# Kernel optimization log

Measured on AMD Instinct MI355X. Metric: run time of the kernel, lower is better.

The kernel has to match this reference:

```python
import jax, jax.numpy as jnp
import numpy as np

N = 50000
E = 500000
CH = 256
H1, C1 = 4, 64
H2, C2 = 8, 32
CONCAT = H1 * C1 + H2 * C2  # 512


def setup_inputs() -> dict:
    key = jax.random.key(0)
    ks = jax.random.split(key, 16)
    s = 0.05
    x = jax.random.normal(ks[0], (N, CH), dtype=jnp.float32)
    edge_index = jax.random.randint(ks[1], (2, E), 0, N, dtype=jnp.int64)
    return {
        "x": x,
        "edge_index": edge_index,
        "gamma": jnp.ones((CH,), jnp.float32),
        "beta": jnp.zeros((CH,), jnp.float32),
        "W1": jax.random.normal(ks[2], (CH, H1 * C1), jnp.float32) * s,
        "a_src1": jax.random.normal(ks[3], (H1, C1), jnp.float32) * s,
        "a_dst1": jax.random.normal(ks[4], (H1, C1), jnp.float32) * s,
        "b1": jnp.zeros((H1 * C1,), jnp.float32),
        "W2": jax.random.normal(ks[5], (CH, H2 * C2), jnp.float32) * s,
        "a_src2": jax.random.normal(ks[6], (H2, C2), jnp.float32) * s,
        "a_dst2": jax.random.normal(ks[7], (H2, C2), jnp.float32) * s,
        "b2": jnp.zeros((H2 * C2,), jnp.float32),
        "Wu": jax.random.normal(ks[8], (CONCAT, CH), jnp.float32) * s,
        "bu": jnp.zeros((CH,), jnp.float32),
    }


def _layer_norm(x, gamma, beta, eps=1e-5):
    mu = jnp.mean(x, axis=-1, keepdims=True)
    var = jnp.var(x, axis=-1, keepdims=True)
    return (x - mu) * jax.lax.rsqrt(var + eps) * gamma + beta


def _gat_conv(x, src, dst, W, a_src, a_dst, bias, heads, out_ch, n_nodes):
    # x: [N, CH] -> per-head projection h: [N, H, C]
    h = (x @ W).reshape(n_nodes, heads, out_ch)
    alpha_s = jnp.einsum('nhc,hc->nh', h, a_src)  # [N, H]
    alpha_d = jnp.einsum('nhc,hc->nh', h, a_dst)  # [N, H]
    e = jax.nn.leaky_relu(alpha_s[src] + alpha_d[dst], negative_slope=0.2)  # [E, H]
    # segment softmax over incoming edges of each dst node (self-loops guarantee nonempty segments)
    m = jax.ops.segment_max(e, dst, num_segments=n_nodes)
    ex = jnp.exp(e - m[dst])
    denom = jax.ops.segment_sum(ex, dst, num_segments=n_nodes)
    a = ex / (denom[dst] + 1e-16)  # [E, H]
    msg = h[src] * a[:, :, None]  # [E, H, C]
    out = jax.ops.segment_sum(msg, dst, num_segments=n_nodes)  # [N, H, C]
    return out.reshape(n_nodes, heads * out_ch) + bias


def reference(x, edge_index, gamma, beta, W1, a_src1, a_dst1, b1,
              W2, a_src2, a_dst2, b2, Wu, bu):
    n = x.shape[0]
    # add self-loops (PyG GATConv default)
    loop = jnp.arange(n, dtype=edge_index.dtype)
    src = jnp.concatenate([edge_index[0], loop])
    dst = jnp.concatenate([edge_index[1], loop])

    residual = x
    x_norm = _layer_norm(x, gamma, beta)
    out1 = _gat_conv(x_norm, src, dst, W1, a_src1, a_dst1, b1, H1, C1, n)
    out2 = _gat_conv(x_norm, src, dst, W2, a_src2, a_dst2, b2, H2, C2, n)
    x_cat = jax.nn.elu(jnp.concatenate([out1, out2], axis=-1))
    unified = x_cat @ Wu + bu
    return residual + unified
```

## Files before the change

### kernel.cpp

```cpp
#include <hip/hip_runtime.h>
#include <hip/hip_bf16.h>
#include <math.h>

constexpr int CH = 256;
constexpr int CC = 512;
constexpr int AP = 16;

typedef __bf16 bf16x8 __attribute__((ext_vector_type(8)));
typedef float  f32x4  __attribute__((ext_vector_type(4)));
typedef float  f32x2  __attribute__((ext_vector_type(2)));
typedef int    i32x4  __attribute__((ext_vector_type(4)));
typedef __attribute__((address_space(3))) void lds_void;
typedef __attribute__((address_space(1))) void glb_void;

__device__ inline unsigned short f2bf(float f) {
    union { float f; unsigned u; } v; v.f = f;
    unsigned r = v.u + 0x7FFFu + ((v.u >> 16) & 1u);
    return (unsigned short)(r >> 16);
}

__global__ void fused_pre_kernel(const float* __restrict__ x, const float* __restrict__ gamma,
                                 const float* __restrict__ beta,
                                 const float* __restrict__ W1, const float* __restrict__ W2,
                                 const float* __restrict__ Wu,
                                 unsigned short* __restrict__ xnb,
                                 unsigned short* __restrict__ WT1, unsigned short* __restrict__ WTu,
                                 int* __restrict__ deg, int N, int LNB) {
    int b = blockIdx.x;
    int t = threadIdx.x;
    if (b < LNB) {
        int wid = b * 4 + (t >> 6);
        int lane = t & 63;
        if (wid >= N) return;
        const float4 v = *(const float4*)(x + (size_t)wid * CH + lane * 4);
        float s = v.x + v.y + v.z + v.w;
        float sq = v.x * v.x + v.y * v.y + v.z * v.z + v.w * v.w;
        #pragma unroll
        for (int o = 32; o; o >>= 1) { s += __shfl_xor(s, o); sq += __shfl_xor(sq, o); }
        float mu = s * (1.0f / CH);
        float var = sq * (1.0f / CH) - mu * mu;
        float rs = rsqrtf(var + 1e-5f);
        float4 g = *(const float4*)(gamma + lane * 4);
        float4 bb = *(const float4*)(beta + lane * 4);
        unsigned short o0 = f2bf((v.x - mu) * rs * g.x + bb.x);
        unsigned short o1 = f2bf((v.y - mu) * rs * g.y + bb.y);
        unsigned short o2 = f2bf((v.z - mu) * rs * g.z + bb.z);
        unsigned short o3 = f2bf((v.w - mu) * rs * g.w + bb.w);
        uint2 pk;
        pk.x = (unsigned)o0 | ((unsigned)o1 << 16);
        pk.y = (unsigned)o2 | ((unsigned)o3 << 16);
        *(uint2*)(xnb + (size_t)wid * CH + lane * 4) = pk;
    } else if (b < LNB + 512) {
        int idx = (b - LNB) * 256 + t;
        int n = idx >> 8, k = idx & 255;
        float v = (n < 256) ? W1[(size_t)k * 256 + n] : W2[(size_t)k * 256 + (n - 256)];
        WT1[idx] = f2bf(v);
    } else if (b < LNB + 1024) {
        int idx = (b - LNB - 512) * 256 + t;
        int n = idx >> 9, k = idx & 511;
        WTu[idx] = f2bf(Wu[(size_t)k * 256 + n]);
    } else {
        int i = (b - LNB - 1024) * 256 + t;
        if (i < N) deg[i] = 1;
    }
}

__device__ inline void gemm_core(const unsigned short* __restrict__ Ab,
                                 const unsigned short* __restrict__ Bt,
                                 unsigned short* As, unsigned short* Bs,
                                 f32x4 acc[4][4], int m0, int n0, int M, int K) {
    const int t = threadIdx.x;
    const int lane = t & 63;
    const int wave = t >> 6;
    const int wr = wave >> 1, wc = wave & 1;
    const int srow = lane >> 3;
    const int scol = (((lane & 7) ^ srow) << 3);
    const int fr = lane & 15;
    const int fkb = (lane >> 4) << 4;

    for (int k0 = 0; k0 < K; k0 += 64) {
        __syncthreads();
        #pragma unroll
        for (int c = 0; c < 4; ++c) {
            int chunk = c * 4 + wave;
            int row = chunk * 8 + srow;
            int gra = m0 + row; if (gra >= M) gra = M - 1;
            const unsigned short* ga = Ab + (size_t)gra * K + k0 + scol;
            __builtin_amdgcn_global_load_lds((const glb_void*)ga,
                                             (lds_void*)&As[chunk * 512], 16, 0, 0);
            const unsigned short* gb = Bt + (size_t)(n0 + row) * K + k0 + scol;
            __builtin_amdgcn_global_load_lds((const glb_void*)gb,
                                             (lds_void*)&Bs[chunk * 512], 16, 0, 0);
        }
        __syncthreads();
        #pragma unroll
        for (int ks = 0; ks < 2; ++ks) {
            bf16x8 af[4], bfr[4];
            #pragma unroll
            for (int m = 0; m < 4; ++m) {
                int r = wr * 64 + m * 16 + fr;
                int cb = (ks * 64 + fkb) ^ ((r & 7) << 4);
                af[m] = *(const bf16x8*)((const char*)As + r * 128 + cb);
            }
            #pragma unroll
            for (int n = 0; n < 4; ++n) {
                int r = wc * 64 + n * 16 + fr;
                int cb = (ks * 64 + fkb) ^ ((r & 7) << 4);
                bfr[n] = *(const bf16x8*)((const char*)Bs + r * 128 + cb);
            }
            #pragma unroll
            for (int m = 0; m < 4; ++m)
                #pragma unroll
                for (int n = 0; n < 4; ++n)
                    acc[m][n] = __builtin_amdgcn_mfma_f32_16x16x32_bf16(af[m], bfr[n], acc[m][n], 0, 0, 0);
        }
    }
}

__global__ __launch_bounds__(256) void gemm1_mfma(
    const unsigned short* __restrict__ Ab, const unsigned short* __restrict__ Bt,
    const float* __restrict__ as1, const float* __restrict__ ad1,
    const float* __restrict__ as2, const float* __restrict__ ad2,
    unsigned char* __restrict__ Hq,
    float* __restrict__ alpha_src, float* __restrict__ alpha_dst, int M, int MB) {
    __shared__ unsigned short As[128 * 64];
    __shared__ unsigned short Bs[128 * 64];
    const int s = blockIdx.x;
    const int xcd = s & 7;
    const int jj = s >> 3;
    const int n_blk = jj & 3;
    const int m_blk = (jj >> 2) * 8 + xcd;
    if (m_blk >= MB) return;
    const int m0 = m_blk * 128, n0 = n_blk * 128;
    const int lane = threadIdx.x & 63;
    const int wave = threadIdx.x >> 6;
    const int wr = wave >> 1, wc = wave & 1;
    f32x4 acc[4][4] = {};
    gemm_core(Ab, Bt, As, Bs, acc, m0, n0, M, 256);
    const int fr = lane & 15;
    const int orow = (lane >> 4) * 4;
    #pragma unroll
    for (int m = 0; m < 4; ++m)
        #pragma unroll
        for (int j = 0; j < 4; ++j) {
            int r = m0 + wr * 64 + m * 16 + orow + j;
            if (r < M) {
                #pragma unroll
                for (int n = 0; n < 4; ++n) {
                    int ccol = n0 + wc * 64 + n * 16 + fr;
                    unsigned q = (unsigned)__builtin_amdgcn_cvt_pk_fp8_f32(
                        acc[m][n][j], acc[m][n][j], 0, false) & 0xffu;
                    Hq[(size_t)r * CC + ccol] = (unsigned char)q;
                }
            }
        }
    const int colbase = n0 + wc * 64;
    const bool gat1 = colbase < 256;
    float sv[4], dv[4];
    int headA;
    if (gat1) {
        headA = colbase >> 6;
        #pragma unroll
        for (int n = 0; n < 4; ++n) { int c = colbase + n * 16 + fr; sv[n] = as1[c]; dv[n] = ad1[c]; }
    } else {
        headA = 4 + ((colbase - 256) >> 5);
        #pragma unroll
        for (int n = 0; n < 4; ++n) { int c = colbase - 256 + n * 16 + fr; sv[n] = as2[c]; dv[n] = ad2[c]; }
    }
    #pragma unroll
    for (int m = 0; m < 4; ++m)
        #pragma unroll
        for (int j = 0; j < 4; ++j) {
            int r = m0 + wr * 64 + m * 16 + orow + j;
            float p01s = acc[m][0][j] * sv[0] + acc[m][1][j] * sv[1];
            float p23s = acc[m][2][j] * sv[2] + acc[m][3][j] * sv[3];
            float p01d = acc[m][0][j] * dv[0] + acc[m][1][j] * dv[1];
            float p23d = acc[m][2][j] * dv[2] + acc[m][3][j] * dv[3];
            if (gat1) {
                float ts = p01s + p23s, td = p01d + p23d;
                #pragma unroll
                for (int o = 1; o < 16; o <<= 1) { ts += __shfl_xor(ts, o); td += __shfl_xor(td, o); }
                if (fr == 0 && r < M) {
                    alpha_src[(size_t)r * AP + headA] = ts;
                    alpha_dst[(size_t)r * AP + headA] = td;
                }
            } else {
                #pragma unroll
                for (int o = 1; o < 16; o <<= 1) {
                    p01s += __shfl_xor(p01s, o); p23s += __shfl_xor(p23s, o);
                    p01d += __shfl_xor(p01d, o); p23d += __shfl_xor(p23d, o);
                }
                if (fr == 0 && r < M) {
                    alpha_src[(size_t)r * AP + headA]     = p01s;
                    alpha_dst[(size_t)r * AP + headA]     = p01d;
                    alpha_src[(size_t)r * AP + headA + 1] = p23s;
                    alpha_dst[(size_t)r * AP + headA + 1] = p23d;
                }
            }
        }
}

__global__ __launch_bounds__(256) void gemm2_mfma(const unsigned short* __restrict__ Ab,
                                                  const unsigned short* __restrict__ Bt,
                                                  const float* __restrict__ bu,
                                                  const float* __restrict__ xres,
                                                  float* __restrict__ C, int M, int MB) {
    __shared__ unsigned short As[128 * 64];
    __shared__ unsigned short Bs[128 * 64];
    const int s = blockIdx.x;
    const int xcd = s & 7;
    const int jj = s >> 3;
    const int n_blk = jj & 1;
    const int m_blk = (jj >> 1) * 8 + xcd;
    if (m_blk >= MB) return;
    const int m0 = m_blk * 128, n0 = n_blk * 128;
    const int lane = threadIdx.x & 63;
    const int wave = threadIdx.x >> 6;
    const int wr = wave >> 1, wc = wave & 1;
    f32x4 acc[4][4] = {};
    gemm_core(Ab, Bt, As, Bs, acc, m0, n0, M, 512);
    const int fr = lane & 15;
    const int orow = (lane >> 4) * 4;
    #pragma unroll
    for (int m = 0; m < 4; ++m)
        #pragma unroll
        for (int j = 0; j < 4; ++j) {
            int r = m0 + wr * 64 + m * 16 + orow + j;
            if (r < M) {
                #pragma unroll
                for (int n = 0; n < 4; ++n) {
                    int ccol = n0 + wc * 64 + n * 16 + fr;
                    float xr = __builtin_nontemporal_load(&xres[(size_t)r * CH + ccol]);
                    __builtin_nontemporal_store(acc[m][n][j] + bu[ccol] + xr,
                                                &C[(size_t)r * CH + ccol]);
                }
            }
        }
}

__global__ void hist_kernel(const int* __restrict__ dst, int* __restrict__ deg, int E) {
    int i = blockIdx.x * blockDim.x + threadIdx.x;
    if (i < E) atomicAdd(&deg[dst[i]], 1);
}
__global__ __launch_bounds__(256) void scan1_kernel(const int* __restrict__ deg, int* __restrict__ pre,
                                                    int* __restrict__ bsum, int n) {
    __shared__ int wsum[4];
    int t = threadIdx.x, lane = t & 63, w = t >> 6;
    int base = blockIdx.x * 1024 + t * 4;
    int v0 = base     < n ? deg[base]     : 0;
    int v1 = base + 1 < n ? deg[base + 1] : 0;
    int v2 = base + 2 < n ? deg[base + 2] : 0;
    int v3 = base + 3 < n ? deg[base + 3] : 0;
    int s = v0 + v1 + v2 + v3;
    int sc = s;
    #pragma unroll
    for (int o = 1; o < 64; o <<= 1) { int xx = __shfl_up(sc, o); if (lane >= o) sc += xx; }
    if (lane == 63) wsum[w] = sc;
    __syncthreads();
    int wo = 0;
    #pragma unroll
    for (int k = 0; k < 4; ++k) if (k < w) wo += wsum[k];
    int p = wo + sc - s;
    if (base     < n) pre[base]     = p; p += v0;
    if (base + 1 < n) pre[base + 1] = p; p += v1;
    if (base + 2 < n) pre[base + 2] = p; p += v2;
    if (base + 3 < n) pre[base + 3] = p;
    if (t == 255) bsum[blockIdx.x] = wo + sc;
}
__global__ void scan2_kernel(int* __restrict__ bsum, int nb) {
    int lane = threadIdx.x;
    int v = lane < nb ? bsum[lane] : 0;
    int sc = v;
    #pragma unroll
    for (int o = 1; o < 64; o <<= 1) { int xx = __shfl_up(sc, o); if (lane >= o) sc += xx; }
    if (lane < nb) bsum[lane] = sc - v;
}
__global__ void scan3_csr_kernel(const int* __restrict__ pre, const int* __restrict__ bsum,
                                 int* __restrict__ offsets, int* __restrict__ cursor,
                                 int* __restrict__ csr, int n, int total) {
    int i = blockIdx.x * 256 + threadIdx.x;
    if (i < n) {
        int off = pre[i] + bsum[i >> 10];
        offsets[i] = off;
        cursor[i] = off + 1;
        csr[off] = i;
    }
    if (i == 0) offsets[n] = total;
}
__global__ void scatter_kernel(const int* __restrict__ src, const int* __restrict__ dst,
                               int* __restrict__ cursor, int* __restrict__ csr, int E) {
    int i = blockIdx.x * blockDim.x + threadIdx.x;
    if (i < E) {
        int pos = atomicAdd(&cursor[dst[i]], 1);
        csr[pos] = src[i];
    }
}

__global__ void aggregate_kernel(const unsigned char* __restrict__ Hq,
                                 const float* __restrict__ alpha_src,
                                 const float* __restrict__ alpha_dst,
                                 const int* __restrict__ offsets,
                                 const int* __restrict__ csr,
                                 const float* __restrict__ b1, const float* __restrict__ b2,
                                 unsigned short* __restrict__ xcb, int N) {
    int n = (blockIdx.x * blockDim.x + threadIdx.x) >> 6;
    int lane = threadIdx.x & 63;
    if (n >= N) return;
    int beg = offsets[n], end = offsets[n + 1];
    int c0 = lane * 8;
    int hid = (lane < 32) ? (lane >> 3) : (4 + ((lane - 32) >> 2));
    float adh = alpha_dst[(size_t)n * AP + hid];

    float ssum = 0.f;
    float a0 = 0, a1 = 0, a2 = 0, a3 = 0, a4 = 0, a5 = 0, a6 = 0, a7 = 0;

    int i = beg;
    for (; i + 4 <= end; i += 4) {
        int ss[4];
        #pragma unroll
        for (int u = 0; u < 4; ++u) ss[u] = __builtin_nontemporal_load(csr + i + u);
        float lw[4];
        #pragma unroll
        for (int u = 0; u < 4; ++u) lw[u] = alpha_src[(size_t)ss[u] * AP + hid];
        uint2 hv[4];
        #pragma unroll
        for (int u = 0; u < 4; ++u) hv[u] = *(const uint2*)(Hq + (size_t)ss[u] * CC + c0);
        #pragma unroll
        for (int u = 0; u < 4; ++u) {
            float l = lw[u] + adh;
            l = l > 0.f ? l : 0.2f * l;
            float wv = __expf(l);
            ssum += wv;
            f32x2 p0 = __builtin_amdgcn_cvt_pk_f32_fp8(hv[u].x, false);
            f32x2 p1 = __builtin_amdgcn_cvt_pk_f32_fp8(hv[u].x, true);
            f32x2 p2 = __builtin_amdgcn_cvt_pk_f32_fp8(hv[u].y, false);
            f32x2 p3 = __builtin_amdgcn_cvt_pk_f32_fp8(hv[u].y, true);
            a0 += wv * p0[0]; a1 += wv * p0[1];
            a2 += wv * p1[0]; a3 += wv * p1[1];
            a4 += wv * p2[0]; a5 += wv * p2[1];
            a6 += wv * p3[0]; a7 += wv * p3[1];
        }
    }
    for (; i < end; ++i) {
        int s0 = __builtin_nontemporal_load(csr + i);
        float l = alpha_src[(size_t)s0 * AP + hid] + adh;
        uint2 hv0 = *(const uint2*)(Hq + (size_t)s0 * CC + c0);
        l = l > 0.f ? l : 0.2f * l;
        float wv = __expf(l);
        ssum += wv;
        f32x2 p0 = __builtin_amdgcn_cvt_pk_f32_fp8(hv0.x, false);
        f32x2 p1 = __builtin_amdgcn_cvt_pk_f32_fp8(hv0.x, true);
        f32x2 p2 = __builtin_amdgcn_cvt_pk_f32_fp8(hv0.y, false);
        f32x2 p3 = __builtin_amdgcn_cvt_pk_f32_fp8(hv0.y, true);
        a0 += wv * p0[0]; a1 += wv * p0[1];
        a2 += wv * p1[0]; a3 += wv * p1[1];
        a4 += wv * p2[0]; a5 += wv * p2[1];
        a6 += wv * p3[0]; a7 += wv * p3[1];
    }

    float inv = 1.0f / (ssum + 1e-16f);
    const float* bb = (c0 < 256) ? (b1 + c0) : (b2 + (c0 - 256));
    float4 bb0 = *(const float4*)(bb), bb1 = *(const float4*)(bb + 4);
    float o[8];
    o[0] = a0 * inv + bb0.x; o[1] = a1 * inv + bb0.y; o[2] = a2 * inv + bb0.z; o[3] = a3 * inv + bb0.w;
    o[4] = a4 * inv + bb1.x; o[5] = a5 * inv + bb1.y; o[6] = a6 * inv + bb1.z; o[7] = a7 * inv + bb1.w;
    #pragma unroll
    for (int j = 0; j < 8; ++j) o[j] = o[j] > 0.f ? o[j] : expm1f(o[j]);
    unsigned short u[8];
    #pragma unroll
    for (int j = 0; j < 8; ++j) u[j] = f2bf(o[j]);
    i32x4 pk;
    pk[0] = (int)((unsigned)u[0] | ((unsigned)u[1] << 16));
    pk[1] = (int)((unsigned)u[2] | ((unsigned)u[3] << 16));
    pk[2] = (int)((unsigned)u[4] | ((unsigned)u[5] << 16));
    pk[3] = (int)((unsigned)u[6] | ((unsigned)u[7] << 16));
    __builtin_nontemporal_store(pk, (i32x4*)(xcb + (size_t)n * CC + c0));
}

extern "C" void kernel_launch(void* const* d_in, const int* in_sizes, int n_in,
                              void* d_out, int out_size, void* d_ws, size_t ws_size,
                              hipStream_t stream) {
    const float* x     = (const float*)d_in[0];
    const int*   ei    = (const int*)d_in[1];
    const float* gamma = (const float*)d_in[2];
    const float* beta  = (const float*)d_in[3];
    const float* W1    = (const float*)d_in[4];
    const float* as1   = (const float*)d_in[5];
    const float* ad1   = (const float*)d_in[6];
    const float* b1    = (const float*)d_in[7];
    const float* W2    = (const float*)d_in[8];
    const float* as2   = (const float*)d_in[9];
    const float* ad2   = (const float*)d_in[10];
    const float* b2    = (const float*)d_in[11];
    const float* Wu    = (const float*)d_in[12];
    const float* bu    = (const float*)d_in[13];
    float* out = (float*)d_out;

    const int N = in_sizes[0] / CH;
    const int E = in_sizes[1] / 2;
    const int* src = ei;
    const int* dst = ei + E;

    char* w = (char*)d_ws;
    auto alloc = [&](size_t bytes) { char* p = w; w += (bytes + 255) & ~(size_t)255; return p; };
    unsigned char*  Hq  = (unsigned char*)alloc((size_t)N * CC);
    unsigned short* xnb = (unsigned short*)alloc((size_t)N * CH * 2);
    unsigned short* xcb = (unsigned short*)alloc((size_t)N * CC * 2);
    unsigned short* WT1 = (unsigned short*)alloc(512 * 256 * 2);
    unsigned short* WTu = (unsigned short*)alloc(256 * 512 * 2);
    float* alpha_src = (float*)alloc((size_t)N * AP * 4);
    float* alpha_dst = (float*)alloc((size_t)N * AP * 4);
    int* deg     = (int*)alloc((size_t)N * 4);
    int* pre     = (int*)alloc((size_t)N * 4);
    int* bsum    = (int*)alloc(64 * 4);
    int* offsets = (int*)alloc(((size_t)N + 1) * 4);
    int* cursor  = (int*)alloc((size_t)N * 4);
    int* csr     = (int*)alloc(((size_t)E + N) * 4);

    const int LNB = (N + 3) / 4;
    const int DEGB = (N + 255) / 256;
    fused_pre_kernel<<<LNB + 1024 + DEGB, 256, 0, stream>>>(x, gamma, beta, W1, W2, Wu,
                                                            xnb, WT1, WTu, deg, N, LNB);

    const int MB = (N + 127) / 128;
    const int MB8 = ((MB + 7) / 8) * 8;
    gemm1_mfma<<<MB8 * 4, 256, 0, stream>>>(xnb, WT1, as1, ad1, as2, ad2,
                                            Hq, alpha_src, alpha_dst, N, MB);

    hist_kernel<<<(E + 255) / 256, 256, 0, stream>>>(dst, deg, E);
    int nb = (N + 1023) / 1024;
    scan1_kernel<<<nb, 256, 0, stream>>>(deg, pre, bsum, N);
    scan2_kernel<<<1, 64, 0, stream>>>(bsum, nb);
    scan3_csr_kernel<<<(N + 255) / 256, 256, 0, stream>>>(pre, bsum, offsets, cursor, csr, N, E + N);
    scatter_kernel<<<(E + 255) / 256, 256, 0, stream>>>(src, dst, cursor, csr, E);

    aggregate_kernel<<<(N + 3) / 4, 256, 0, stream>>>(Hq, alpha_src, alpha_dst, offsets, csr,
                                                      b1, b2, xcb, N);

    gemm2_mfma<<<MB8 * 2, 256, 0, stream>>>(xcb, WTu, bu, x, out, N, MB);
}
```

Baseline: 221.0 us.

## Double-buffer LDS tiles in GEMM core and reduce alpha via LDS transpose

Rewrites the shared GEMM mainloop so each K-step stages the next tile into a second LDS buffer while MFMAs consume the current one. This removes one barrier per iteration and lets global-to-LDS loads overlap with compute, at the cost of doubling LDS per block, which may lower occupancy. It also replaces the 16-lane shuffle reductions for the attention logits in the gemm1 epilogue with an LDS transpose-and-sum, so each lane writes one row's result.

```diff
diff --git a/kernel.cpp b/kernel.cpp
--- a/kernel.cpp
+++ b/kernel.cpp
@@ -65,10 +65,11 @@
     }
 }
 
-__device__ inline void gemm_core(const unsigned short* __restrict__ Ab,
-                                 const unsigned short* __restrict__ Bt,
-                                 unsigned short* As, unsigned short* Bs,
-                                 f32x4 acc[4][4], int m0, int n0, int M, int K) {
+template<int K>
+__device__ inline void gemm_core_db(const unsigned short* __restrict__ Ab,
+                                    const unsigned short* __restrict__ Bt,
+                                    unsigned short* As, unsigned short* Bs,
+                                    f32x4 acc[4][4], int m0, int n0, int M) {
     const int t = threadIdx.x;
     const int lane = t & 63;
     const int wave = t >> 6;
@@ -78,8 +79,7 @@
     const int fr = lane & 15;
     const int fkb = (lane >> 4) << 4;
 
-    for (int k0 = 0; k0 < K; k0 += 64) {
-        __syncthreads();
+    auto stage = [&](int buf, int k0) {
         #pragma unroll
         for (int c = 0; c < 4; ++c) {
             int chunk = c * 4 + wave;
@@ -87,12 +87,14 @@
             int gra = m0 + row; if (gra >= M) gra = M - 1;
             const unsigned short* ga = Ab + (size_t)gra * K + k0 + scol;
             __builtin_amdgcn_global_load_lds((const glb_void*)ga,
-                                             (lds_void*)&As[chunk * 512], 16, 0, 0);
+                                             (lds_void*)&As[buf * 8192 + chunk * 512], 16, 0, 0);
             const unsigned short* gb = Bt + (size_t)(n0 + row) * K + k0 + scol;
             __builtin_amdgcn_global_load_lds((const glb_void*)gb,
-                                             (lds_void*)&Bs[chunk * 512], 16, 0, 0);
+                                             (lds_void*)&Bs[buf * 8192 + chunk * 512], 16, 0, 0);
         }
-        __syncthreads();
+    };
+    auto compute = [&](int buf) {
+        const int bb = buf * 16384;
         #pragma unroll
         for (int ks = 0; ks < 2; ++ks) {
             bf16x8 af[4], bfr[4];
@@ -100,13 +102,13 @@
             for (int m = 0; m < 4; ++m) {
                 int r = wr * 64 + m * 16 + fr;
                 int cb = (ks * 64 + fkb) ^ ((r & 7) << 4);
-                af[m] = *(const bf16x8*)((const char*)As + r * 128 + cb);
+                af[m] = *(const bf16x8*)((const char*)As + bb + r * 128 + cb);
             }
             #pragma unroll
             for (int n = 0; n < 4; ++n) {
                 int r = wc * 64 + n * 16 + fr;
                 int cb = (ks * 64 + fkb) ^ ((r & 7) << 4);
-                bfr[n] = *(const bf16x8*)((const char*)Bs + r * 128 + cb);
+                bfr[n] = *(const bf16x8*)((const char*)Bs + bb + r * 128 + cb);
             }
             #pragma unroll
             for (int m = 0; m < 4; ++m)
@@ -114,7 +116,19 @@
                 for (int n = 0; n < 4; ++n)
                     acc[m][n] = __builtin_amdgcn_mfma_f32_16x16x32_bf16(af[m], bfr[n], acc[m][n], 0, 0, 0);
         }
-    }
+    };
+
+    stage(0, 0);
+    __syncthreads();
+    int cur = 0;
+    #pragma unroll
+    for (int k0 = 64; k0 < K; k0 += 64) {
+        stage(cur ^ 1, k0);
+        compute(cur);
+        __syncthreads();
+        cur ^= 1;
+    }
+    compute(cur);
 }
 
 __global__ __launch_bounds__(256) void gemm1_mfma(
@@ -123,8 +137,8 @@
     const float* __restrict__ as2, const float* __restrict__ ad2,
     unsigned char* __restrict__ Hq,
     float* __restrict__ alpha_src, float* __restrict__ alpha_dst, int M, int MB) {
-    __shared__ unsigned short As[128 * 64];
-    __shared__ unsigned short Bs[128 * 64];
+    __shared__ unsigned short As[2 * 128 * 64];
+    __shared__ unsigned short Bs[2 * 128 * 64];
     const int s = blockIdx.x;
     const int xcd = s & 7;
     const int jj = s >> 3;
@@ -136,7 +150,7 @@
     const int wave = threadIdx.x >> 6;
     const int wr = wave >> 1, wc = wave & 1;
     f32x4 acc[4][4] = {};
-    gemm_core(Ab, Bt, As, Bs, acc, m0, n0, M, 256);
+    gemm_core_db<256>(Ab, Bt, As, Bs, acc, m0, n0, M);
     const int fr = lane & 15;
     const int orow = (lane >> 4) * 4;
     #pragma unroll
@@ -156,48 +170,61 @@
         }
     const int colbase = n0 + wc * 64;
     const bool gat1 = colbase < 256;
-    float sv[4], dv[4];
+    f32x4 svv, dvv;
     int headA;
     if (gat1) {
         headA = colbase >> 6;
         #pragma unroll
-        for (int n = 0; n < 4; ++n) { int c = colbase + n * 16 + fr; sv[n] = as1[c]; dv[n] = ad1[c]; }
+        for (int n = 0; n < 4; ++n) { int c = colbase + n * 16 + fr; svv[n] = as1[c]; dvv[n] = ad1[c]; }
     } else {
         headA = 4 + ((colbase - 256) >> 5);
         #pragma unroll
-        for (int n = 0; n < 4; ++n) { int c = colbase - 256 + n * 16 + fr; sv[n] = as2[c]; dv[n] = ad2[c]; }
-    }
-    #pragma unroll
-    for (int m = 0; m < 4; ++m)
-        #pragma unroll
-        for (int j = 0; j < 4; ++j) {
-            int r = m0 + wr * 64 + m * 16 + orow + j;
-            float p01s = acc[m][0][j] * sv[0] + acc[m][1][j] * sv[1];
-            float p23s = acc[m][2][j] * sv[2] + acc[m][3][j] * sv[3];
-            float p01d = acc[m][0][j] * dv[0] + acc[m][1][j] * dv[1];
-            float p23d = acc[m][2][j] * dv[2] + acc[m][3][j] * dv[3];
-            if (gat1) {
-                float ts = p01s + p23s, td = p01d + p23d;
-                #pragma unroll
-                for (int o = 1; o < 16; o <<= 1) { ts += __shfl_xor(ts, o); td += __shfl_xor(td, o); }
-                if (fr == 0 && r < M) {
-                    alpha_src[(size_t)r * AP + headA] = ts;
-                    alpha_dst[(size_t)r * AP + headA] = td;
-                }
-            } else {
-                #pragma unroll
-                for (int o = 1; o < 16; o <<= 1) {
-                    p01s += __shfl_xor(p01s, o); p23s += __shfl_xor(p23s, o);
-                    p01d += __shfl_xor(p01d, o); p23d += __shfl_xor(p23d, o);
-                }
-                if (fr == 0 && r < M) {
-                    alpha_src[(size_t)r * AP + headA]     = p01s;
-                    alpha_dst[(size_t)r * AP + headA]     = p01d;
-                    alpha_src[(size_t)r * AP + headA + 1] = p23s;
-                    alpha_dst[(size_t)r * AP + headA + 1] = p23d;
-                }
-            }
-        }
+        for (int n = 0; n < 4; ++n) { int c = colbase - 256 + n * 16 + fr; svv[n] = as2[c]; dvv[n] = ad2[c]; }
+    }
+    __syncthreads();
+    float* S = (float*)As + wave * 1024;
+    const int g = lane >> 4, kslot = lane & 15;
+    const int rown = m0 + wr * 64 + (kslot >> 2) * 16 + g * 4 + (kslot & 3);
+    const bool rok = rown < M;
+    auto xpose_reduce = [&](f32x4 q0, f32x4 q1, f32x4 q2, f32x4 q3) -> float {
+        float* base = S + lane * 16;
+        *(f32x4*)(base + 0)  = q0;
+        *(f32x4*)(base + 4)  = q1;
+        *(f32x4*)(base + 8)  = q2;
+        *(f32x4*)(base + 12) = q3;
+        const float* rb = S + g * 256 + kslot;
+        float sum = 0.f;
+        #pragma unroll
+        for (int f = 0; f < 16; ++f) sum += rb[f * 16];
+        return sum;
+    };
+    #define PARTF(m, j, W)  (acc[m][0][j]*W[0] + acc[m][1][j]*W[1] + acc[m][2][j]*W[2] + acc[m][3][j]*W[3])
+    #define PART01(m, j, W) (acc[m][0][j]*W[0] + acc[m][1][j]*W[1])
+    #define PART23(m, j, W) (acc[m][2][j]*W[2] + acc[m][3][j]*W[3])
+    #define QUADF(m, W)  (f32x4){PARTF(m,0,W), PARTF(m,1,W), PARTF(m,2,W), PARTF(m,3,W)}
+    #define QUAD01(m, W) (f32x4){PART01(m,0,W), PART01(m,1,W), PART01(m,2,W), PART01(m,3,W)}
+    #define QUAD23(m, W) (f32x4){PART23(m,0,W), PART23(m,1,W), PART23(m,2,W), PART23(m,3,W)}
+    if (gat1) {
+        float ts = xpose_reduce(QUADF(0, svv), QUADF(1, svv), QUADF(2, svv), QUADF(3, svv));
+        if (rok) alpha_src[(size_t)rown * AP + headA] = ts;
+        float td = xpose_reduce(QUADF(0, dvv), QUADF(1, dvv), QUADF(2, dvv), QUADF(3, dvv));
+        if (rok) alpha_dst[(size_t)rown * AP + headA] = td;
+    } else {
+        float s01 = xpose_reduce(QUAD01(0, svv), QUAD01(1, svv), QUAD01(2, svv), QUAD01(3, svv));
+        if (rok) alpha_src[(size_t)rown * AP + headA] = s01;
+        float s23 = xpose_reduce(QUAD23(0, svv), QUAD23(1, svv), QUAD23(2, svv), QUAD23(3, svv));
+        if (rok) alpha_src[(size_t)rown * AP + headA + 1] = s23;
+        float d01 = xpose_reduce(QUAD01(0, dvv), QUAD01(1, dvv), QUAD01(2, dvv), QUAD01(3, dvv));
+        if (rok) alpha_dst[(size_t)rown * AP + headA] = d01;
+        float d23 = xpose_reduce(QUAD23(0, dvv), QUAD23(1, dvv), QUAD23(2, dvv), QUAD23(3, dvv));
+        if (rok) alpha_dst[(size_t)rown * AP + headA + 1] = d23;
+    }
+    #undef PARTF
+    #undef PART01
+    #undef PART23
+    #undef QUADF
+    #undef QUAD01
+    #undef QUAD23
 }
 
 __global__ __launch_bounds__(256) void gemm2_mfma(const unsigned short* __restrict__ Ab,
@@ -205,8 +232,8 @@
                                                   const float* __restrict__ bu,
                                                   const float* __restrict__ xres,
                                                   float* __restrict__ C, int M, int MB) {
-    __shared__ unsigned short As[128 * 64];
-    __shared__ unsigned short Bs[128 * 64];
+    __shared__ unsigned short As[2 * 128 * 64];
+    __shared__ unsigned short Bs[2 * 128 * 64];
     const int s = blockIdx.x;
     const int xcd = s & 7;
     const int jj = s >> 3;
@@ -218,7 +245,7 @@
     const int wave = threadIdx.x >> 6;
     const int wr = wave >> 1, wc = wave & 1;
     f32x4 acc[4][4] = {};
-    gemm_core(Ab, Bt, As, Bs, acc, m0, n0, M, 512);
+    gemm_core_db<512>(Ab, Bt, As, Bs, acc, m0, n0, M);
     const int fr = lane & 15;
     const int orow = (lane >> 4) * 4;
     #pragma unroll
```

New measurement: 212.7 us. 1.04x faster.
